# Kernel optimization log

Measured on AMD Instinct MI355X. Metric: run time of the kernel, lower is better.

The kernel has to match this reference:

```python
import jax, jax.numpy as jnp
import numpy as np

L, B, D = 1024, 4, 1024
E, K, H = 8, 2, 4096


def setup_inputs() -> dict:
    key = jax.random.key(0)
    ks = jax.random.split(key, 12)
    s_g = 1.0 / np.sqrt(D)
    s_h = 1.0 / np.sqrt(H)
    return {
        "inputs": jax.random.normal(ks[0], (L, B, D), jnp.float32),
        "task_param": jax.random.normal(ks[1], (B, D), jnp.float32),
        "gate_img_w": jax.random.normal(ks[2], (D, E), jnp.float32) * s_g,
        "gate_img_b": jnp.zeros((E,), jnp.float32),
        "gate_txt_w": jax.random.normal(ks[3], (D, E), jnp.float32) * s_g,
        "gate_txt_b": jnp.zeros((E,), jnp.float32),
        "task_gate_w": jax.random.normal(ks[4], (D, E), jnp.float32) * s_g,
        "task_gate_b": jnp.zeros((E,), jnp.float32),
        "alpha": jnp.float32(0.5),
        "w1": jax.random.normal(ks[5], (E, D, H), jnp.float32) * s_g,
        "w2": jax.random.normal(ks[6], (E, H, D), jnp.float32) * s_h,
        "is_text": 1,
    }


def reference(inputs, task_param, gate_img_w, gate_img_b, gate_txt_w, gate_txt_b,
              task_gate_w, task_gate_b, alpha, w1, w2, is_text):
    # task gate: (B, E) -> broadcast over L
    task_logits = (task_param @ task_gate_w + task_gate_b)[None]  # (1, B, E)
    if is_text:
        input_logits = inputs @ gate_txt_w + gate_txt_b  # (L, B, E)
    else:
        input_logits = inputs @ gate_img_w + gate_img_b
    gate_logits = (1.0 - alpha) * input_logits + alpha * task_logits  # (L, B, E)

    topk_vals, sel = jax.lax.top_k(gate_logits, K)  # (L, B, K)

    # auxiliary load-balancing loss
    soft = jax.nn.softmax(gate_logits.astype(jnp.float32), axis=-1)
    avg_weight = soft.mean(axis=(0, 1))                       # (E,)
    expert_mask = jax.nn.one_hot(sel, E).sum(axis=2)          # (L, B, E)
    avg_count = expert_mask.mean(axis=(0, 1))                 # (E,)
    l_aux = jnp.mean(avg_weight * avg_count) * E

    # renormalized top-k weights, combined per expert: (L, B, E)
    weights = jax.nn.softmax(topk_vals.astype(jnp.float32), axis=-1).astype(inputs.dtype)
    comb = jnp.sum(jax.nn.one_hot(sel, E, dtype=weights.dtype) * weights[..., None], axis=2)

    # dense per-expert FFN, weighted combine (loop over fixed small E)
    results = jnp.zeros_like(inputs)
    for e in range(E):
        h = jax.nn.gelu(inputs @ w1[e])      # (L, B, H)
        out = h @ w2[e]                      # (L, B, D)
        results = results + comb[..., e:e + 1] * out
    return results, l_aux.astype(jnp.float32)
```

## Files before the change

### kernel.cpp

```cpp
#include <hip/hip_runtime.h>
#include <hip/hip_bf16.h>
#include <math.h>

#define L_ 1024
#define B_ 4
#define D_ 1024
#define E_ 8
#define K_ 2
#define H_ 4096
#define T_ (L_*B_)
#define P_ (T_*K_)
#define PPAD (P_+256)

typedef unsigned short u16;
typedef __attribute__((ext_vector_type(4))) float f32x4;
typedef __attribute__((ext_vector_type(8))) short s16x8;

__device__ __forceinline__ u16 f2bf(float f) {
  uint32_t u = __float_as_uint(f);
  uint32_t r = (u + 0x7FFFu + ((u >> 16) & 1u)) >> 16;
  return (u16)r;
}
__device__ __forceinline__ float gelu_fast(float v) {
  float u = v * (1.0f + 0.044715f * v * v);
  float t = __expf(-1.5957691216057308f * u);
  return v / (1.0f + t);
}

template<int R, int C>
__global__ void convtrans(const float* __restrict__ in, u16* __restrict__ out) {
  __shared__ float tile[64][65];
  int e = blockIdx.z;
  int r0 = blockIdx.y * 64, c0 = blockIdx.x * 64;
  const float* src = in + (size_t)e * R * C;
  u16* dst = out + (size_t)e * R * C;
  int t = threadIdx.x;
  int tr = t >> 4, tc = (t & 15) * 4;
#pragma unroll
  for (int p = 0; p < 4; ++p) {
    int r = tr + p * 16;
    float4 v = *(const float4*)(src + (size_t)(r0 + r) * C + c0 + tc);
    tile[r][tc] = v.x; tile[r][tc+1] = v.y; tile[r][tc+2] = v.z; tile[r][tc+3] = v.w;
  }
  __syncthreads();
#pragma unroll
  for (int p = 0; p < 4; ++p) {
    int c = tr + p * 16;
    ushort4 o;
    o.x = f2bf(tile[tc+0][c]); o.y = f2bf(tile[tc+1][c]);
    o.z = f2bf(tile[tc+2][c]); o.w = f2bf(tile[tc+3][c]);
    *(ushort4*)(dst + (size_t)(c0 + c) * R + r0 + tc) = o;
  }
}

__global__ void gating(const float* __restrict__ x, const float* __restrict__ task_param,
                       const float* __restrict__ gw_img, const float* __restrict__ gb_img,
                       const float* __restrict__ gw_txt, const float* __restrict__ gb_txt,
                       const float* __restrict__ tgw, const float* __restrict__ tgb,
                       const float* __restrict__ alpha_p, const int* __restrict__ is_text_p,
                       float4* __restrict__ sel_w, float* __restrict__ prob_part,
                       int* __restrict__ count_part) {
  __shared__ float wprob[4][8];
  __shared__ int wcnt[4][8];
  int wid = threadIdx.x >> 6, lane = threadIdx.x & 63;
  int t = blockIdx.x * 4 + wid;
  int b = t & (B_ - 1);
  int it = is_text_p[0];
  const float* gw = it ? gw_txt : gw_img;
  const float* gb = it ? gb_txt : gb_img;
  float alpha = alpha_p[0];
  const float* xr = x + (size_t)t * D_;
  const float* tp = task_param + (size_t)b * D_;
  float acc[8] = {0,0,0,0,0,0,0,0};
  float tac[8] = {0,0,0,0,0,0,0,0};
  for (int i = 0; i < D_/64; ++i) {
    int d = i * 64 + lane;
    float xv = xr[d], tv = tp[d];
#pragma unroll
    for (int e = 0; e < 8; ++e) {
      acc[e] += xv * gw[d*8 + e];
      tac[e] += tv * tgw[d*8 + e];
    }
  }
#pragma unroll
  for (int e = 0; e < 8; ++e) {
#pragma unroll
    for (int off = 32; off > 0; off >>= 1) {
      acc[e] += __shfl_xor(acc[e], off);
      tac[e] += __shfl_xor(tac[e], off);
    }
  }
  float lg[8];
#pragma unroll
  for (int e = 0; e < 8; ++e)
    lg[e] = (1.0f - alpha) * (acc[e] + gb[e]) + alpha * (tac[e] + tgb[e]);
  float m = lg[0];
#pragma unroll
  for (int e = 1; e < 8; ++e) m = fmaxf(m, lg[e]);
  float pr[8], ps = 0.f;
#pragma unroll
  for (int e = 0; e < 8; ++e) { pr[e] = expf(lg[e] - m); ps += pr[e]; }
  float inv = 1.0f / ps;
  int i0 = 0; float v0 = lg[0];
#pragma unroll
  for (int e = 1; e < 8; ++e) if (lg[e] > v0) { v0 = lg[e]; i0 = e; }
  int i1 = -1; float v1 = -1e30f;
#pragma unroll
  for (int e = 0; e < 8; ++e) if (e != i0 && lg[e] > v1) { v1 = lg[e]; i1 = e; }
  float ex = expf(v1 - v0);
  float w0 = 1.0f / (1.0f + ex), w1 = ex / (1.0f + ex);
  if (lane == 0) {
    sel_w[t] = make_float4(__int_as_float(i0), __int_as_float(i1), w0, w1);
#pragma unroll
    for (int e = 0; e < 8; ++e) {
      wprob[wid][e] = pr[e] * inv;
      wcnt[wid][e] = (i0 == e) + (i1 == e);
    }
  }
  __syncthreads();
  if (threadIdx.x < 8) {
    int e = threadIdx.x;
    prob_part[blockIdx.x * 8 + e] = wprob[0][e] + wprob[1][e] + wprob[2][e] + wprob[3][e];
    count_part[blockIdx.x * 8 + e] = wcnt[0][e] + wcnt[1][e] + wcnt[2][e] + wcnt[3][e];
  }
}

__global__ void finalize(const float* __restrict__ prob_part, const int* __restrict__ count_part,
                         int* __restrict__ counts, int* __restrict__ offs,
                         int* __restrict__ cursors, float* __restrict__ laux_out) {
  __shared__ float ps_[256];
  __shared__ int cs_[256];
  int t = threadIdx.x;
  int e = t & 7, s = t >> 3;
  float p = 0.f; int c = 0;
  for (int b = s; b < 1024; b += 32) { p += prob_part[b*8 + e]; c += count_part[b*8 + e]; }
  ps_[t] = p; cs_[t] = c;
  __syncthreads();
  for (int st = 16; st > 0; st >>= 1) {
    if (s < st) { ps_[t] += ps_[t + st*8]; cs_[t] += cs_[t + st*8]; }
    __syncthreads();
  }
  if (t == 0) {
    int off = 0; float laux = 0.f;
    for (int ee = 0; ee < 8; ++ee) {
      int cnt = cs_[ee];
      counts[ee] = cnt; offs[ee] = off; cursors[ee] = off; off += cnt;
      laux += (ps_[ee] * (1.0f/4096.0f)) * ((float)cnt * (1.0f/4096.0f));
    }
    *laux_out = laux;
  }
}

__global__ void scatter_gather(const float* __restrict__ x, const float4* __restrict__ sel_w,
                               int* __restrict__ cursors, float* __restrict__ pair_w,
                               int* __restrict__ pair_idx, u16* __restrict__ Xg) {
  int wid = threadIdx.x >> 6, lane = threadIdx.x & 63;
  int t = blockIdx.x * 4 + wid;
  float4 sw = sel_w[t];
  int s0 = __float_as_int(sw.x), s1 = __float_as_int(sw.y);
  int p0 = 0, p1 = 0;
  if (lane == 0) {
    p0 = atomicAdd(&cursors[s0], 1);
    p1 = atomicAdd(&cursors[s1], 1);
  }
  p0 = __shfl(p0, 0); p1 = __shfl(p1, 0);
  if (lane == 0) {
    pair_w[p0] = sw.z; pair_w[p1] = sw.w;
    pair_idx[t*2] = p0; pair_idx[t*2+1] = p1;
  }
  const float* xr = x + (size_t)t * D_;
  u16* d0 = Xg + (size_t)p0 * D_;
  u16* d1 = Xg + (size_t)p1 * D_;
#pragma unroll
  for (int i = 0; i < 4; ++i) {
    int c = i * 256 + lane * 4;
    float4 v = *(const float4*)(xr + c);
    ushort4 o;
    o.x = f2bf(v.x); o.y = f2bf(v.y); o.z = f2bf(v.z); o.w = f2bf(v.w);
    *(ushort4*)(d0 + c) = o;
    *(ushort4*)(d1 + c) = o;
  }
}

template<int EPI, int KDIM, int KLEN, int NOUT, int NPANEL, int KSPLIT, int JSLOTS>
__global__ __launch_bounds__(512, 2)
void gemm256(const u16* __restrict__ Tok, const u16* __restrict__ Wt,
             const int* __restrict__ counts, const int* __restrict__ offs,
             const float* __restrict__ pair_w,
             u16* __restrict__ Hout, float* __restrict__ Cout) {
  int gid = blockIdx.x;
  int e = gid & 7;
  int idx = gid >> 3;
  int panel = idx % NPANEL; idx /= NPANEL;
  int ks = idx % KSPLIT;    idx /= KSPLIT;
  int j0 = idx;
  int ne = counts[e];
  int off = offs[e];
  int kbase = ks * KLEN;
  float* Cpart = Cout + (size_t)ks * P_ * D_;

  __shared__ u16 As[2][16384];
  __shared__ u16 Bs[2][16384];
  int t = threadIdx.x, lane = t & 63, wid = t >> 6;
  int wf = wid & 1, wt = wid >> 1;

  const u16* Wg = Wt + (size_t)e * NOUT * KDIM + (size_t)panel * 256 * KDIM + kbase;

  int rowoff[4]; int ldsoff[4];
#pragma unroll
  for (int i = 0; i < 4; ++i) {
    int slot = i * 512 + t;
    int row = slot >> 3;
    int kk = (slot & 7) ^ (row & 7);
    rowoff[i] = row * KDIM + kk * 8;
    ldsoff[i] = slot * 8;
  }

  int aoff[8][2], boff[4][2];
#pragma unroll
  for (int r = 0; r < 8; ++r) {
    int row = wf * 128 + r * 16 + (lane & 15);
#pragma unroll
    for (int h = 0; h < 2; ++h) {
      int kk = h * 4 + (lane >> 4);
      aoff[r][h] = (row * 8 + (kk ^ (row & 7))) * 8;
    }
  }
#pragma unroll
  for (int f = 0; f < 4; ++f) {
    int row = wt * 64 + f * 16 + (lane & 15);
#pragma unroll
    for (int h = 0; h < 2; ++h) {
      int kk = h * 4 + (lane >> 4);
      boff[f][h] = (row * 8 + (kk ^ (row & 7))) * 8;
    }
  }

  constexpr int NT = KLEN / 64;
  int lr = lane & 15, lg4 = (lane >> 4) * 4;

  for (int bx = j0; bx * 256 < ne; bx += JSLOTS) {
    const u16* Tg = Tok + (size_t)(off + bx * 256) * KDIM + kbase;
    f32x4 acc[8][4] = {};
#pragma unroll
    for (int i = 0; i < 4; ++i) {
      __builtin_amdgcn_global_load_lds(
          (const __attribute__((address_space(1))) void*)(Wg + rowoff[i]),
          (__attribute__((address_space(3))) void*)(&As[0][ldsoff[i]]), 16, 0, 0);
      __builtin_amdgcn_global_load_lds(
          (const __attribute__((address_space(1))) void*)(Tg + rowoff[i]),
          (__attribute__((address_space(3))) void*)(&Bs[0][ldsoff[i]]), 16, 0, 0);
    }
    __syncthreads();
    int cur = 0;
    for (int tt = 0; tt < NT; ++tt) {
      if (tt + 1 < NT) {
        int k0 = (tt + 1) * 64;
        int nb = cur ^ 1;
#pragma unroll
        for (int i = 0; i < 4; ++i) {
          __builtin_amdgcn_global_load_lds(
              (const __attribute__((address_space(1))) void*)(Wg + rowoff[i] + k0),
              (__attribute__((address_space(3))) void*)(&As[nb][ldsoff[i]]), 16, 0, 0);
          __builtin_amdgcn_global_load_lds(
              (const __attribute__((address_space(1))) void*)(Tg + rowoff[i] + k0),
              (__attribute__((address_space(3))) void*)(&Bs[nb][ldsoff[i]]), 16, 0, 0);
        }
      }
      const u16* Ab = &As[cur][0]; const u16* Bb = &Bs[cur][0];
#pragma unroll
      for (int h = 0; h < 2; ++h) {
        s16x8 a[8], b[4];
#pragma unroll
        for (int r = 0; r < 8; ++r) a[r] = *(const s16x8*)(Ab + aoff[r][h]);
#pragma unroll
        for (int f = 0; f < 4; ++f) b[f] = *(const s16x8*)(Bb + boff[f][h]);
#pragma unroll
        for (int r = 0; r < 8; ++r)
#pragma unroll
          for (int f = 0; f < 4; ++f)
            acc[r][f] = __builtin_amdgcn_mfma_f32_16x16x32_bf16(a[r], b[f], acc[r][f], 0, 0, 0);
      }
      __syncthreads();
      cur ^= 1;
    }

#pragma unroll
    for (int f = 0; f < 4; ++f) {
      int tokl = bx * 256 + wt * 64 + f * 16 + lr;
      if (tokl >= ne) continue;
      size_t grow = (size_t)(off + tokl);
      if (EPI == 0) {
#pragma unroll
        for (int r = 0; r < 8; ++r) {
          ushort4 o;
          o.x = f2bf(gelu_fast(acc[r][f][0]));
          o.y = f2bf(gelu_fast(acc[r][f][1]));
          o.z = f2bf(gelu_fast(acc[r][f][2]));
          o.w = f2bf(gelu_fast(acc[r][f][3]));
          *(ushort4*)(Hout + grow * NOUT + panel * 256 + wf * 128 + r * 16 + lg4) = o;
        }
      } else {
        float w = pair_w[grow];
#pragma unroll
        for (int r = 0; r < 8; ++r) {
          float4 o;
          o.x = acc[r][f][0] * w; o.y = acc[r][f][1] * w;
          o.z = acc[r][f][2] * w; o.w = acc[r][f][3] * w;
          *(float4*)(Cpart + grow * NOUT + panel * 256 + wf * 128 + r * 16 + lg4) = o;
        }
      }
    }
  }
}

__global__ void combine(const float* __restrict__ pair_out, const int* __restrict__ pair_idx,
                        float* __restrict__ out) {
  const float* part1 = pair_out + (size_t)P_ * D_;
  int t = blockIdx.x;
  int p0 = pair_idx[t*2], p1 = pair_idx[t*2+1];
  int c = threadIdx.x * 4;
  float4 a0 = *(const float4*)(pair_out + (size_t)p0 * D_ + c);
  float4 a1 = *(const float4*)(part1    + (size_t)p0 * D_ + c);
  float4 b0 = *(const float4*)(pair_out + (size_t)p1 * D_ + c);
  float4 b1 = *(const float4*)(part1    + (size_t)p1 * D_ + c);
  float4 o;
  o.x = (a0.x + a1.x) + (b0.x + b1.x);
  o.y = (a0.y + a1.y) + (b0.y + b1.y);
  o.z = (a0.z + a1.z) + (b0.z + b1.z);
  o.w = (a0.w + a1.w) + (b0.w + b1.w);
  *(float4*)(out + (size_t)t * D_ + c) = o;
}

extern "C" void kernel_launch(void* const* d_in, const int* in_sizes, int n_in,
                              void* d_out, int out_size, void* d_ws, size_t ws_size,
                              hipStream_t stream) {
  const float* inputs      = (const float*)d_in[0];
  const float* task_param  = (const float*)d_in[1];
  const float* gate_img_w  = (const float*)d_in[2];
  const float* gate_img_b  = (const float*)d_in[3];
  const float* gate_txt_w  = (const float*)d_in[4];
  const float* gate_txt_b  = (const float*)d_in[5];
  const float* task_gate_w = (const float*)d_in[6];
  const float* task_gate_b = (const float*)d_in[7];
  const float* alpha       = (const float*)d_in[8];
  const float* w1          = (const float*)d_in[9];
  const float* w2          = (const float*)d_in[10];
  const int*   is_text     = (const int*)d_in[11];
  float* out = (float*)d_out;

  char* ws = (char*)d_ws;
  u16* w1b = (u16*)(ws + 0);
  u16* w2b = (u16*)(ws + 67108864);
  u16* Xg  = (u16*)(ws + 134217728);
  u16* Hb  = (u16*)(ws + 151519232);
  float4* sel_w   = (float4*)(ws + 220725248);
  float* pair_w   = (float*)(ws + 220725248 + 65536);
  int* pair_idx   = (int*)(ws + 220725248 + 98816);
  float* prob_part= (float*)(ws + 220725248 + 131584);
  int* count_part = (int*)(ws + 220725248 + 164352);
  int* counters   = (int*)(ws + 220725248 + 197120);
  float* pair_out = (float*)(ws + 0);

  int* counts  = counters;
  int* offs    = counters + 8;
  int* cursors = counters + 16;

  convtrans<D_, H_><<<dim3(H_/64, D_/64, E_), 256, 0, stream>>>(w1, w1b);
  convtrans<H_, D_><<<dim3(D_/64, H_/64, E_), 256, 0, stream>>>(w2, w2b);
  gating<<<dim3(T_/4), 256, 0, stream>>>(inputs, task_param, gate_img_w, gate_img_b,
      gate_txt_w, gate_txt_b, task_gate_w, task_gate_b, alpha, is_text,
      sel_w, prob_part, count_part);
  finalize<<<dim3(1), 256, 0, stream>>>(prob_part, count_part, counts, offs, cursors,
      out + (size_t)T_ * D_);
  scatter_gather<<<dim3(T_/4), 256, 0, stream>>>(inputs, sel_w, cursors, pair_w, pair_idx, Xg);
  gemm256<0, D_, D_, H_, 16, 1, 2><<<dim3(256), 512, 0, stream>>>(
      Xg, w1b, counts, offs, pair_w, Hb, (float*)nullptr);
  gemm256<1, H_, H_/2, D_, 4, 2, 4><<<dim3(256), 512, 0, stream>>>(
      Hb, w2b, counts, offs, pair_w, (u16*)nullptr, pair_out);
  combine<<<dim3(T_), 256, 0, stream>>>(pair_out, pair_idx, out);
}
```

Before: 512.5 us.

## Replace double-buffered K loop with 4-stage ring of 32-wide K slices

The expert GEMM main loop moves from a two-buffer scheme with 64-wide K tiles to a four-slot LDS ring of 32-wide K slices, keeping three slices in flight. Explicit vmcnt/lgkmcnt waits and a single barrier per slice replace the two __syncthreads per tile, and s_setprio raises wave priority around the MFMA block. The LDS swizzle is redone for the narrower 4-chunk rows. The goal is to hide more global-load latency behind the matrix math and cut synchronization overhead. In exchange the hand-written wait counts become fragile, and the smaller slices mean fewer MFMAs per barrier.

Measured after the change: 584.5 us. 1.14x slower.

```diff
diff --git a/kernel.cpp b/kernel.cpp
--- a/kernel.cpp
+++ b/kernel.cpp
@@ -199,91 +199,101 @@
   int kbase = ks * KLEN;
   float* Cpart = Cout + (size_t)ks * P_ * D_;
 
-  __shared__ u16 As[2][16384];
-  __shared__ u16 Bs[2][16384];
+  __shared__ u16 As[4][8192];
+  __shared__ u16 Bs[4][8192];
   int t = threadIdx.x, lane = t & 63, wid = t >> 6;
   int wf = wid & 1, wt = wid >> 1;
 
   const u16* Wg = Wt + (size_t)e * NOUT * KDIM + (size_t)panel * 256 * KDIM + kbase;
 
-  int rowoff[4]; int ldsoff[4];
-#pragma unroll
-  for (int i = 0; i < 4; ++i) {
+  int goff[2], ldso[2];
+#pragma unroll
+  for (int i = 0; i < 2; ++i) {
     int slot = i * 512 + t;
-    int row = slot >> 3;
-    int kk = (slot & 7) ^ (row & 7);
-    rowoff[i] = row * KDIM + kk * 8;
-    ldsoff[i] = slot * 8;
-  }
-
-  int aoff[8][2], boff[4][2];
-#pragma unroll
-  for (int r = 0; r < 8; ++r) {
-    int row = wf * 128 + r * 16 + (lane & 15);
-#pragma unroll
-    for (int h = 0; h < 2; ++h) {
-      int kk = h * 4 + (lane >> 4);
-      aoff[r][h] = (row * 8 + (kk ^ (row & 7))) * 8;
-    }
-  }
-#pragma unroll
-  for (int f = 0; f < 4; ++f) {
-    int row = wt * 64 + f * 16 + (lane & 15);
-#pragma unroll
-    for (int h = 0; h < 2; ++h) {
-      int kk = h * 4 + (lane >> 4);
-      boff[f][h] = (row * 8 + (kk ^ (row & 7))) * 8;
-    }
-  }
-
-  constexpr int NT = KLEN / 64;
+    int r = slot >> 2;
+    int p = slot & 3;
+    int kk = p ^ (r & 3) ^ ((r >> 2) & 3);
+    goff[i] = r * KDIM + kk * 8;
+    ldso[i] = slot * 8;
+  }
+
+  int aoff[8], boff[4];
+#pragma unroll
+  for (int fr = 0; fr < 8; ++fr) {
+    int row = wf * 128 + fr * 16 + (lane & 15);
+    int p = (lane >> 4) ^ (row & 3) ^ ((row >> 2) & 3);
+    aoff[fr] = (row * 4 + p) * 8;
+  }
+#pragma unroll
+  for (int fb = 0; fb < 4; ++fb) {
+    int row = wt * 64 + fb * 16 + (lane & 15);
+    int p = (lane >> 4) ^ (row & 3) ^ ((row >> 2) & 3);
+    boff[fb] = (row * 4 + p) * 8;
+  }
+
+  constexpr int NS = KLEN / 32;
   int lr = lane & 15, lg4 = (lane >> 4) * 4;
 
   for (int bx = j0; bx * 256 < ne; bx += JSLOTS) {
     const u16* Tg = Tok + (size_t)(off + bx * 256) * KDIM + kbase;
     f32x4 acc[8][4] = {};
-#pragma unroll
-    for (int i = 0; i < 4; ++i) {
-      __builtin_amdgcn_global_load_lds(
-          (const __attribute__((address_space(1))) void*)(Wg + rowoff[i]),
-          (__attribute__((address_space(3))) void*)(&As[0][ldsoff[i]]), 16, 0, 0);
-      __builtin_amdgcn_global_load_lds(
-          (const __attribute__((address_space(1))) void*)(Tg + rowoff[i]),
-          (__attribute__((address_space(3))) void*)(&Bs[0][ldsoff[i]]), 16, 0, 0);
-    }
-    __syncthreads();
-    int cur = 0;
-    for (int tt = 0; tt < NT; ++tt) {
-      if (tt + 1 < NT) {
-        int k0 = (tt + 1) * 64;
-        int nb = cur ^ 1;
-#pragma unroll
-        for (int i = 0; i < 4; ++i) {
-          __builtin_amdgcn_global_load_lds(
-              (const __attribute__((address_space(1))) void*)(Wg + rowoff[i] + k0),
-              (__attribute__((address_space(3))) void*)(&As[nb][ldsoff[i]]), 16, 0, 0);
-          __builtin_amdgcn_global_load_lds(
-              (const __attribute__((address_space(1))) void*)(Tg + rowoff[i] + k0),
-              (__attribute__((address_space(3))) void*)(&Bs[nb][ldsoff[i]]), 16, 0, 0);
-        }
-      }
-      const u16* Ab = &As[cur][0]; const u16* Bb = &Bs[cur][0];
-#pragma unroll
-      for (int h = 0; h < 2; ++h) {
-        s16x8 a[8], b[4];
-#pragma unroll
-        for (int r = 0; r < 8; ++r) a[r] = *(const s16x8*)(Ab + aoff[r][h]);
-#pragma unroll
-        for (int f = 0; f < 4; ++f) b[f] = *(const s16x8*)(Bb + boff[f][h]);
-#pragma unroll
-        for (int r = 0; r < 8; ++r)
-#pragma unroll
-          for (int f = 0; f < 4; ++f)
-            acc[r][f] = __builtin_amdgcn_mfma_f32_16x16x32_bf16(a[r], b[f], acc[r][f], 0, 0, 0);
-      }
-      __syncthreads();
-      cur ^= 1;
-    }
+
+#define STAGE(sl)                                                              \
+    {                                                                          \
+      int ring_ = (sl) & 3;                                                    \
+      int ko_ = (sl) * 32;                                                     \
+      _Pragma("unroll")                                                        \
+      for (int i_ = 0; i_ < 2; ++i_) {                                         \
+        __builtin_amdgcn_global_load_lds(                                      \
+            (const __attribute__((address_space(1))) void*)(Wg + goff[i_] + ko_), \
+            (__attribute__((address_space(3))) void*)(&As[ring_][ldso[i_]]), 16, 0, 0); \
+        __builtin_amdgcn_global_load_lds(                                      \
+            (const __attribute__((address_space(1))) void*)(Tg + goff[i_] + ko_), \
+            (__attribute__((address_space(3))) void*)(&Bs[ring_][ldso[i_]]), 16, 0, 0); \
+      }                                                                        \
+    }
+
+#define COMPSL(sl)                                                             \
+    {                                                                          \
+      const u16* Ab_ = &As[(sl) & 3][0];                                       \
+      const u16* Bb_ = &Bs[(sl) & 3][0];                                       \
+      s16x8 a_[8], b_[4];                                                      \
+      _Pragma("unroll")                                                        \
+      for (int r_ = 0; r_ < 8; ++r_) a_[r_] = *(const s16x8*)(Ab_ + aoff[r_]); \
+      _Pragma("unroll")                                                        \
+      for (int f_ = 0; f_ < 4; ++f_) b_[f_] = *(const s16x8*)(Bb_ + boff[f_]); \
+      asm volatile("s_waitcnt lgkmcnt(0)" ::: "memory");                       \
+      __builtin_amdgcn_sched_barrier(0);                                       \
+      __builtin_amdgcn_s_setprio(1);                                           \
+      _Pragma("unroll")                                                        \
+      for (int r_ = 0; r_ < 8; ++r_)                                           \
+        _Pragma("unroll")                                                      \
+        for (int f_ = 0; f_ < 4; ++f_)                                         \
+          acc[r_][f_] = __builtin_amdgcn_mfma_f32_16x16x32_bf16(               \
+              a_[r_], b_[f_], acc[r_][f_], 0, 0, 0);                           \
+      __builtin_amdgcn_s_setprio(0);                                           \
+    }
+
+    STAGE(0); STAGE(1); STAGE(2);
+    asm volatile("s_waitcnt vmcnt(8)" ::: "memory");
+    __builtin_amdgcn_s_barrier();
+
+    int s = 0;
+    for (; s + 3 < NS; ++s) {
+      STAGE(s + 3);
+      COMPSL(s);
+      asm volatile("s_waitcnt vmcnt(8)" ::: "memory");
+      __builtin_amdgcn_s_barrier();
+    }
+    COMPSL(NS - 3);
+    asm volatile("s_waitcnt vmcnt(0)" ::: "memory");
+    __builtin_amdgcn_s_barrier();
+    COMPSL(NS - 2);
+    COMPSL(NS - 1);
+    __builtin_amdgcn_s_barrier();
+
+#undef STAGE
+#undef COMPSL
 
 #pragma unroll
     for (int f = 0; f < 4; ++f) {
```

## Rewrite grouped GEMM main loop as phased ping-pong pipeline with fine-grained waits

Applied to the files above, without the earlier changes.

Replaces the simple double-buffered K loop with an unrolled two-tile schedule split into four phases per tile. Each phase issues a slice of the next global-to-LDS loads, reads a subset of A fragments, and runs its MFMAs at raised priority. Manual vmcnt/lgkmcnt waits and s_barriers replace full __syncthreads. The aim is to overlap memory traffic with matrix math and reduce barrier stalls, at the cost of fragile hand-tuned wait counts and redundant clamped loads at the tail.

Measured after the change: 514.3 us. Within noise of the previous version (+0.4%).

```diff
diff --git a/kernel.cpp b/kernel.cpp
--- a/kernel.cpp
+++ b/kernel.cpp
@@ -206,14 +206,14 @@
 
   const u16* Wg = Wt + (size_t)e * NOUT * KDIM + (size_t)panel * 256 * KDIM + kbase;
 
-  int rowoff[4]; int ldsoff[4];
+  int goff[4]; int ldso[4];
 #pragma unroll
   for (int i = 0; i < 4; ++i) {
     int slot = i * 512 + t;
     int row = slot >> 3;
     int kk = (slot & 7) ^ (row & 7);
-    rowoff[i] = row * KDIM + kk * 8;
-    ldsoff[i] = slot * 8;
+    goff[i] = row * KDIM + kk * 8;
+    ldso[i] = slot * 8;
   }
 
   int aoff[8][2], boff[4][2];
@@ -237,52 +237,82 @@
   }
 
   constexpr int NT = KLEN / 64;
+  constexpr int NITER = NT / 2;
   int lr = lane & 15, lg4 = (lane >> 4) * 4;
+
+#define STA(b, q, tk) __builtin_amdgcn_global_load_lds( \
+      (const __attribute__((address_space(1))) void*)(Wg + goff[q] + (tk) * 64), \
+      (__attribute__((address_space(3))) void*)(&As[b][ldso[q]]), 16, 0, 0)
+#define STB(b, q, tk) __builtin_amdgcn_global_load_lds( \
+      (const __attribute__((address_space(1))) void*)(Tg + goff[q] + (tk) * 64), \
+      (__attribute__((address_space(3))) void*)(&Bs[b][ldso[q]]), 16, 0, 0)
+
+#define PH(MP, TB, DOB, VM, LG8, ...)                                          \
+  {                                                                            \
+    s16x8 a00 = *(const s16x8*)(&As[TB][aoff[(MP)*2+0][0]]);                   \
+    s16x8 a01 = *(const s16x8*)(&As[TB][aoff[(MP)*2+0][1]]);                   \
+    s16x8 a10 = *(const s16x8*)(&As[TB][aoff[(MP)*2+1][0]]);                   \
+    s16x8 a11 = *(const s16x8*)(&As[TB][aoff[(MP)*2+1][1]]);                   \
+    if (DOB) {                                                                 \
+      _Pragma("unroll")                                                        \
+      for (int nf = 0; nf < 4; ++nf) {                                         \
+        bn[nf][0] = *(const s16x8*)(&Bs[TB][boff[nf][0]]);                     \
+        bn[nf][1] = *(const s16x8*)(&Bs[TB][boff[nf][1]]);                     \
+      }                                                                        \
+    }                                                                          \
+    __VA_ARGS__;                                                               \
+    if (LG8) asm volatile("s_waitcnt lgkmcnt(8)" ::: "memory");                \
+    __builtin_amdgcn_s_barrier();                                              \
+    asm volatile("s_waitcnt lgkmcnt(0)" ::: "memory");                         \
+    __builtin_amdgcn_sched_barrier(0);                                         \
+    __builtin_amdgcn_s_setprio(1);                                             \
+    _Pragma("unroll")                                                          \
+    for (int nf = 0; nf < 4; ++nf) {                                           \
+      acc[(MP)*2+0][nf] = __builtin_amdgcn_mfma_f32_16x16x32_bf16(             \
+          a00, bn[nf][0], acc[(MP)*2+0][nf], 0, 0, 0);                         \
+      acc[(MP)*2+1][nf] = __builtin_amdgcn_mfma_f32_16x16x32_bf16(             \
+          a10, bn[nf][0], acc[(MP)*2+1][nf], 0, 0, 0);                         \
+    }                                                                          \
+    _Pragma("unroll")                                                          \
+    for (int nf = 0; nf < 4; ++nf) {                                           \
+      acc[(MP)*2+0][nf] = __builtin_amdgcn_mfma_f32_16x16x32_bf16(             \
+          a01, bn[nf][1], acc[(MP)*2+0][nf], 0, 0, 0);                         \
+      acc[(MP)*2+1][nf] = __builtin_amdgcn_mfma_f32_16x16x32_bf16(             \
+          a11, bn[nf][1], acc[(MP)*2+1][nf], 0, 0, 0);                         \
+    }                                                                          \
+    __builtin_amdgcn_s_setprio(0);                                             \
+    if (VM == 8)  asm volatile("s_waitcnt vmcnt(8)"  ::: "memory");            \
+    if (VM == 10) asm volatile("s_waitcnt vmcnt(10)" ::: "memory");            \
+    __builtin_amdgcn_s_barrier();                                              \
+  }
 
   for (int bx = j0; bx * 256 < ne; bx += JSLOTS) {
     const u16* Tg = Tok + (size_t)(off + bx * 256) * KDIM + kbase;
     f32x4 acc[8][4] = {};
-#pragma unroll
-    for (int i = 0; i < 4; ++i) {
-      __builtin_amdgcn_global_load_lds(
-          (const __attribute__((address_space(1))) void*)(Wg + rowoff[i]),
-          (__attribute__((address_space(3))) void*)(&As[0][ldsoff[i]]), 16, 0, 0);
-      __builtin_amdgcn_global_load_lds(
-          (const __attribute__((address_space(1))) void*)(Tg + rowoff[i]),
-          (__attribute__((address_space(3))) void*)(&Bs[0][ldsoff[i]]), 16, 0, 0);
-    }
-    __syncthreads();
-    int cur = 0;
-    for (int tt = 0; tt < NT; ++tt) {
-      if (tt + 1 < NT) {
-        int k0 = (tt + 1) * 64;
-        int nb = cur ^ 1;
-#pragma unroll
-        for (int i = 0; i < 4; ++i) {
-          __builtin_amdgcn_global_load_lds(
-              (const __attribute__((address_space(1))) void*)(Wg + rowoff[i] + k0),
-              (__attribute__((address_space(3))) void*)(&As[nb][ldsoff[i]]), 16, 0, 0);
-          __builtin_amdgcn_global_load_lds(
-              (const __attribute__((address_space(1))) void*)(Tg + rowoff[i] + k0),
-              (__attribute__((address_space(3))) void*)(&Bs[nb][ldsoff[i]]), 16, 0, 0);
-        }
-      }
-      const u16* Ab = &As[cur][0]; const u16* Bb = &Bs[cur][0];
-#pragma unroll
-      for (int h = 0; h < 2; ++h) {
-        s16x8 a[8], b[4];
-#pragma unroll
-        for (int r = 0; r < 8; ++r) a[r] = *(const s16x8*)(Ab + aoff[r][h]);
-#pragma unroll
-        for (int f = 0; f < 4; ++f) b[f] = *(const s16x8*)(Bb + boff[f][h]);
-#pragma unroll
-        for (int r = 0; r < 8; ++r)
-#pragma unroll
-          for (int f = 0; f < 4; ++f)
-            acc[r][f] = __builtin_amdgcn_mfma_f32_16x16x32_bf16(a[r], b[f], acc[r][f], 0, 0, 0);
-      }
-      __syncthreads();
-      cur ^= 1;
+    s16x8 bn[4][2];
+
+    STB(0, 0, 0); STB(0, 1, 0);
+    STB(0, 2, 0); STB(0, 3, 0);
+    STA(0, 0, 0); STA(0, 2, 0);
+    STA(0, 1, 0); STA(0, 3, 0);
+    STB(1, 0, 1); STB(1, 1, 1);
+    STB(1, 2, 1); STB(1, 3, 1);
+    STA(1, 0, 1); STA(1, 2, 1);
+    asm volatile("s_waitcnt vmcnt(8)" ::: "memory");
+    __builtin_amdgcn_s_barrier();
+
+    for (int j = 0; j < NITER; ++j) {
+      int t1 = 2 * j + 1;
+      int tc2 = (2 * j + 2 < NT) ? 2 * j + 2 : NT - 1;
+      int tc3 = (2 * j + 3 < NT) ? 2 * j + 3 : NT - 1;
+      PH(0, 0, 1,  0, 1, STA(1, 1, t1); STA(1, 3, t1));
+      PH(1, 0, 0, 10, 0, STB(0, 0, tc2); STB(0, 1, tc2));
+      PH(2, 0, 0,  0, 0, STB(0, 2, tc2); STB(0, 3, tc2));
+      PH(3, 0, 0,  8, 0, STA(0, 0, tc2); STA(0, 2, tc2));
+      PH(0, 1, 1,  0, 1, STA(0, 1, tc2); STA(0, 3, tc2));
+      PH(1, 1, 0, 10, 0, STB(1, 0, tc3); STB(1, 1, tc3));
+      PH(2, 1, 0,  0, 0, STB(1, 2, tc3); STB(1, 3, tc3));
+      PH(3, 1, 0,  8, 0, STA(1, 0, tc3); STA(1, 2, tc3));
     }
 
 #pragma unroll
@@ -312,6 +342,9 @@
       }
     }
   }
+#undef PH
+#undef STA
+#undef STB
 }
 
 __global__ void combine(const float* __restrict__ pair_out, const int* __restrict__ pair_idx,
```

## Halve GEMM K-tile to 32 and raise occupancy to four blocks per CU

Applied to the files above, without the earlier changes.

Shrinks the per-stage K tile in the grouped expert GEMM from 64 to 32, halving LDS usage (64KB to 32KB per block) and reworking the XOR swizzle for 4-chunk rows. Launch bounds go to 4 blocks per CU and the grid doubles to 512 blocks with twice the job slots, aiming to hide latency with more resident waves. In exchange there are twice as many barriers per unit of work and less MFMA work per sync. The 4-block launch bound may also force register spills given the 128 f32 accumulators per thread.

After: 1.456 ms. 2.84x slower.

```diff
diff --git a/kernel.cpp b/kernel.cpp
--- a/kernel.cpp
+++ b/kernel.cpp
@@ -183,7 +183,7 @@
 }
 
 template<int EPI, int KDIM, int KLEN, int NOUT, int NPANEL, int KSPLIT, int JSLOTS>
-__global__ __launch_bounds__(512, 2)
+__global__ __launch_bounds__(512, 4)
 void gemm256(const u16* __restrict__ Tok, const u16* __restrict__ Wt,
              const int* __restrict__ counts, const int* __restrict__ offs,
              const float* __restrict__ pair_w,
@@ -199,88 +199,80 @@
   int kbase = ks * KLEN;
   float* Cpart = Cout + (size_t)ks * P_ * D_;
 
-  __shared__ u16 As[2][16384];
-  __shared__ u16 Bs[2][16384];
+  __shared__ u16 As[2][8192];
+  __shared__ u16 Bs[2][8192];
   int t = threadIdx.x, lane = t & 63, wid = t >> 6;
   int wf = wid & 1, wt = wid >> 1;
 
   const u16* Wg = Wt + (size_t)e * NOUT * KDIM + (size_t)panel * 256 * KDIM + kbase;
 
-  int rowoff[4]; int ldsoff[4];
-#pragma unroll
-  for (int i = 0; i < 4; ++i) {
+  int goff[2], ldso[2];
+#pragma unroll
+  for (int i = 0; i < 2; ++i) {
     int slot = i * 512 + t;
-    int row = slot >> 3;
-    int kk = (slot & 7) ^ (row & 7);
-    rowoff[i] = row * KDIM + kk * 8;
-    ldsoff[i] = slot * 8;
-  }
-
-  int aoff[8][2], boff[4][2];
+    int row = slot >> 2;
+    int p = slot & 3;
+    int kk = p ^ ((row >> 1) & 3);
+    goff[i] = row * KDIM + kk * 8;
+    ldso[i] = slot * 8;
+  }
+
+  int aoff[8], boff[4];
 #pragma unroll
   for (int r = 0; r < 8; ++r) {
     int row = wf * 128 + r * 16 + (lane & 15);
-#pragma unroll
-    for (int h = 0; h < 2; ++h) {
-      int kk = h * 4 + (lane >> 4);
-      aoff[r][h] = (row * 8 + (kk ^ (row & 7))) * 8;
-    }
+    int p = (lane >> 4) ^ ((row >> 1) & 3);
+    aoff[r] = (row * 4 + p) * 8;
   }
 #pragma unroll
   for (int f = 0; f < 4; ++f) {
     int row = wt * 64 + f * 16 + (lane & 15);
-#pragma unroll
-    for (int h = 0; h < 2; ++h) {
-      int kk = h * 4 + (lane >> 4);
-      boff[f][h] = (row * 8 + (kk ^ (row & 7))) * 8;
-    }
-  }
-
-  constexpr int NT = KLEN / 64;
+    int p = (lane >> 4) ^ ((row >> 1) & 3);
+    boff[f] = (row * 4 + p) * 8;
+  }
+
+  constexpr int NT = KLEN / 32;
   int lr = lane & 15, lg4 = (lane >> 4) * 4;
 
   for (int bx = j0; bx * 256 < ne; bx += JSLOTS) {
     const u16* Tg = Tok + (size_t)(off + bx * 256) * KDIM + kbase;
     f32x4 acc[8][4] = {};
 #pragma unroll
-    for (int i = 0; i < 4; ++i) {
+    for (int i = 0; i < 2; ++i) {
       __builtin_amdgcn_global_load_lds(
-          (const __attribute__((address_space(1))) void*)(Wg + rowoff[i]),
-          (__attribute__((address_space(3))) void*)(&As[0][ldsoff[i]]), 16, 0, 0);
+          (const __attribute__((address_space(1))) void*)(Wg + goff[i]),
+          (__attribute__((address_space(3))) void*)(&As[0][ldso[i]]), 16, 0, 0);
       __builtin_amdgcn_global_load_lds(
-          (const __attribute__((address_space(1))) void*)(Tg + rowoff[i]),
-          (__attribute__((address_space(3))) void*)(&Bs[0][ldsoff[i]]), 16, 0, 0);
+          (const __attribute__((address_space(1))) void*)(Tg + goff[i]),
+          (__attribute__((address_space(3))) void*)(&Bs[0][ldso[i]]), 16, 0, 0);
     }
     __syncthreads();
     int cur = 0;
     for (int tt = 0; tt < NT; ++tt) {
       if (tt + 1 < NT) {
-        int k0 = (tt + 1) * 64;
+        int k0 = (tt + 1) * 32;
         int nb = cur ^ 1;
 #pragma unroll
-        for (int i = 0; i < 4; ++i) {
+        for (int i = 0; i < 2; ++i) {
           __builtin_amdgcn_global_load_lds(
-              (const __attribute__((address_space(1))) void*)(Wg + rowoff[i] + k0),
-              (__attribute__((address_space(3))) void*)(&As[nb][ldsoff[i]]), 16, 0, 0);
+              (const __attribute__((address_space(1))) void*)(Wg + goff[i] + k0),
+              (__attribute__((address_space(3))) void*)(&As[nb][ldso[i]]), 16, 0, 0);
           __builtin_amdgcn_global_load_lds(
-              (const __attribute__((address_space(1))) void*)(Tg + rowoff[i] + k0),
-              (__attribute__((address_space(3))) void*)(&Bs[nb][ldsoff[i]]), 16, 0, 0);
+              (const __attribute__((address_space(1))) void*)(Tg + goff[i] + k0),
+              (__attribute__((address_space(3))) void*)(&Bs[nb][ldso[i]]), 16, 0, 0);
         }
       }
       const u16* Ab = &As[cur][0]; const u16* Bb = &Bs[cur][0];
-#pragma unroll
-      for (int h = 0; h < 2; ++h) {
-        s16x8 a[8], b[4];
-#pragma unroll
-        for (int r = 0; r < 8; ++r) a[r] = *(const s16x8*)(Ab + aoff[r][h]);
-#pragma unroll
-        for (int f = 0; f < 4; ++f) b[f] = *(const s16x8*)(Bb + boff[f][h]);
-#pragma unroll
-        for (int r = 0; r < 8; ++r)
-#pragma unroll
-          for (int f = 0; f < 4; ++f)
-            acc[r][f] = __builtin_amdgcn_mfma_f32_16x16x32_bf16(a[r], b[f], acc[r][f], 0, 0, 0);
-      }
+      s16x8 a[8], b[4];
+#pragma unroll
+      for (int r = 0; r < 8; ++r) a[r] = *(const s16x8*)(Ab + aoff[r]);
+#pragma unroll
+      for (int f = 0; f < 4; ++f) b[f] = *(const s16x8*)(Bb + boff[f]);
+#pragma unroll
+      for (int r = 0; r < 8; ++r)
+#pragma unroll
+        for (int f = 0; f < 4; ++f)
+          acc[r][f] = __builtin_amdgcn_mfma_f32_16x16x32_bf16(a[r], b[f], acc[r][f], 0, 0, 0);
       __syncthreads();
       cur ^= 1;
     }
@@ -374,9 +366,9 @@
   finalize<<<dim3(1), 256, 0, stream>>>(prob_part, count_part, counts, offs, cursors,
       out + (size_t)T_ * D_);
   scatter_gather<<<dim3(T_/4), 256, 0, stream>>>(inputs, sel_w, cursors, pair_w, pair_idx, Xg);
-  gemm256<0, D_, D_, H_, 16, 1, 2><<<dim3(256), 512, 0, stream>>>(
+  gemm256<0, D_, D_, H_, 16, 1, 4><<<dim3(512), 512, 0, stream>>>(
       Xg, w1b, counts, offs, pair_w, Hb, (float*)nullptr);
-  gemm256<1, H_, H_/2, D_, 4, 2, 4><<<dim3(256), 512, 0, stream>>>(
+  gemm256<1, H_, H_/2, D_, 4, 2, 8><<<dim3(512), 512, 0, stream>>>(
       Hb, w2b, counts, offs, pair_w, (u16*)nullptr, pair_out);
   combine<<<dim3(T_), 256, 0, stream>>>(pair_out, pair_idx, out);
 }
```
